# Performance work log

Hardware: AMD Instinct MI355X
Metric: run time of the kernel (lower is better)

## Reference

```python
import jax, jax.numpy as jnp
import numpy as np

VOCAB = 267735
CUTOFFS = [20000, 40000, 200000, VOCAB]   # module appends vocab_size
CUT_ENDS = [0] + CUTOFFS
D_PROJ = 1024
D_EMBED = 1024
DIV_VAL = 4
N_CLUSTERS = len(CUTOFFS) - 1  # 3
SEQ, BSZ = 128, 4


def _logit(x, W, b, proj):
    # x: [i,b,d_proj]; proj: [d_emb,d_proj]; W: [n,d_emb]; b: [n]
    y = jnp.einsum('ibd,ed->ibe', x, proj)
    return jnp.einsum('ibe,ne->ibn', y, W) + b


def setup_inputs() -> dict:
    key = jax.random.key(0)
    ks = jax.random.split(key, 16)
    inp = {}
    inp['hidden'] = jax.random.normal(ks[0], (SEQ, BSZ, D_PROJ), jnp.float32)
    inp['target'] = jax.random.randint(ks[1], (SEQ, BSZ), 0, VOCAB, dtype=jnp.int32)
    inp['cluster_weight'] = jax.random.normal(ks[2], (N_CLUSTERS, D_EMBED), jnp.float32) * 0.02
    inp['cluster_bias'] = jnp.zeros((N_CLUSTERS,), jnp.float32)
    for i in range(len(CUTOFFS)):
        d_emb_i = D_EMBED // DIV_VAL ** i
        n_i = CUT_ENDS[i + 1] - CUT_ENDS[i]
        inp[f'proj{i}'] = jax.random.normal(ks[3 + 3 * i], (d_emb_i, D_PROJ), jnp.float32) * 0.02
        inp[f'W{i}'] = jax.random.normal(ks[4 + 3 * i], (n_i, d_emb_i), jnp.float32) * 0.02
        inp[f'b{i}'] = jnp.zeros((n_i,), jnp.float32)
    return inp


def reference(hidden, target, cluster_weight, cluster_bias,
              proj0, proj1, proj2, proj3,
              W0, W1, W2, W3, b0, b1, b2, b3):
    projs = [proj0, proj1, proj2, proj3]
    Ws = [W0, W1, W2, W3]
    bs = [b0, b1, b2, b3]
    # head: shortlist tokens + one pseudo-token per tail cluster
    head_W = jnp.concatenate([W0, cluster_weight], axis=0)   # [20003, d_embed]
    head_b = jnp.concatenate([b0, cluster_bias], axis=0)
    head_logprob = jax.nn.log_softmax(_logit(hidden, head_W, head_b, proj0), axis=-1)
    out = [head_logprob[..., :CUTOFFS[0]]]
    for i in range(1, len(CUTOFFS)):
        tail_logprob = jax.nn.log_softmax(_logit(hidden, Ws[i], bs[i], projs[i]), axis=-1)
        # P(token) = P(cluster i | head) * P(token | cluster i)
        out.append(head_logprob[..., CUTOFFS[0] + i - 1, None] + tail_logprob)
    out = jnp.concatenate(out, axis=-1)  # [seq, bsz, vocab] full log-probs
    # Per-cluster boolean_mask + gather + scatter_nd in the original is exactly
    # a gather of the concatenated log-prob at the target id.
    tgt_logprob = jnp.take_along_axis(out, target[..., None].astype(jnp.int32), axis=-1)[..., 0]
    loss = -jnp.mean(tgt_logprob)  # return_mean=True
    return out, loss
```

## Files before the change

kernel.cpp:

```cpp
#include <hip/hip_runtime.h>
#include <hip/hip_bf16.h>

#define VOCAB_SZ 267735
#define NROWS 512

typedef __attribute__((ext_vector_type(8))) short bf16x8;
typedef __attribute__((ext_vector_type(4))) float f32x4;

typedef const __attribute__((address_space(1))) unsigned int* gas_u32p;
typedef __attribute__((address_space(3))) unsigned int* las_u32p;

#define GLOAD_LDS16(g, l) \
    __builtin_amdgcn_global_load_lds((gas_u32p)(const void*)(g), (las_u32p)(void*)(l), 16, 0, 0)

enum { MODE_Y = 0, MODE_RW = 1 };

template<int MODE>
__global__ __launch_bounds__(256)
void gemm_k(const __hip_bfloat16* __restrict__ A, int lda, int K,
            const __hip_bfloat16* __restrict__ B,
            int Nmat, int Nsplit,
            const float* __restrict__ bias, const float* __restrict__ bias2,
            float* __restrict__ rowsum,
            float* __restrict__ outp, int Nstore,
            float* __restrict__ clog,
            __hip_bfloat16* __restrict__ yout, int yld, int ywidth)
{
    const int t = threadIdx.x;
    const int col0 = blockIdx.x * 128;
    const int row0 = blockIdx.y * 128;
    const int wid = t >> 6, lane = t & 63, q = lane >> 4, l16 = lane & 15;
    const int wm = wid >> 1, wn = wid & 1;

    __shared__ __hip_bfloat16 sA[128 * 32];
    __shared__ __hip_bfloat16 sB[128 * 32];
    __shared__ float rs[2][128];

    f32x4 acc[4][4];
    f32x4 zf = {0.f, 0.f, 0.f, 0.f};
#pragma unroll
    for (int i = 0; i < 4; i++)
#pragma unroll
        for (int j = 0; j < 4; j++) acc[i][j] = zf;

    const int id0 = t, id1 = 256 + t;
    const __hip_bfloat16* a0 = A + (size_t)(row0 + (id0 >> 2)) * lda + ((id0 & 3) << 3);
    const __hip_bfloat16* a1 = A + (size_t)(row0 + (id1 >> 2)) * lda + ((id1 & 3) << 3);
    const __hip_bfloat16* b0 = B + (size_t)(col0 + (id0 >> 2)) * K + ((id0 & 3) << 3);
    const __hip_bfloat16* b1 = B + (size_t)(col0 + (id1 >> 2)) * K + ((id1 & 3) << 3);
    char* sAb = (char*)sA;
    char* sBb = (char*)sB;
    const bf16x8* sAv = (const bf16x8*)sA;
    const bf16x8* sBv = (const bf16x8*)sB;

    for (int k0 = 0; k0 < K; k0 += 32) {
        __syncthreads();
        GLOAD_LDS16(a0 + k0, sAb + id0 * 16);
        GLOAD_LDS16(a1 + k0, sAb + id1 * 16);
        GLOAD_LDS16(b0 + k0, sBb + id0 * 16);
        GLOAD_LDS16(b1 + k0, sBb + id1 * 16);
        __syncthreads();

        bf16x8 af[4], bfr[4];
#pragma unroll
        for (int i = 0; i < 4; i++) af[i]  = sAv[(wm * 64 + i * 16 + l16) * 4 + q];
#pragma unroll
        for (int j = 0; j < 4; j++) bfr[j] = sBv[(wn * 64 + j * 16 + l16) * 4 + q];
#pragma unroll
        for (int i = 0; i < 4; i++)
#pragma unroll
            for (int j = 0; j < 4; j++)
                acc[i][j] = __builtin_amdgcn_mfma_f32_16x16x32_bf16(af[i], bfr[j], acc[i][j], 0, 0, 0);
    }

    int colg[4];
#pragma unroll
    for (int j = 0; j < 4; j++) colg[j] = col0 + wn * 64 + j * 16 + l16;

    if (MODE == MODE_Y) {
#pragma unroll
        for (int i = 0; i < 4; i++) {
            int rbase = row0 + wm * 64 + i * 16 + q * 4;
#pragma unroll
            for (int j = 0; j < 4; j++) {
                if (colg[j] < ywidth) {
#pragma unroll
                    for (int r = 0; r < 4; r++)
                        yout[(size_t)(rbase + r) * yld + colg[j]] = __float2bfloat16(acc[i][j][r]);
                }
            }
        }
    } else {
        float bv[4]; bool ok[4];
#pragma unroll
        for (int j = 0; j < 4; j++) {
            ok[j] = colg[j] < Nmat;
            bv[j] = colg[j] < Nsplit ? bias[colg[j]] : (ok[j] ? bias2[colg[j] - Nsplit] : 0.f);
        }
#pragma unroll
        for (int i = 0; i < 4; i++) {
            int rbase = row0 + wm * 64 + i * 16 + q * 4;
#pragma unroll
            for (int r = 0; r < 4; r++) {
                int rg = rbase + r;
                float* orow = outp + (size_t)rg * VOCAB_SZ;
                float s = 0.f;
#pragma unroll
                for (int j = 0; j < 4; j++) {
                    if (ok[j]) {
                        float v = acc[i][j][r] + bv[j];
                        s += __expf(v);
                        if (colg[j] < Nstore)
                            __builtin_nontemporal_store(v, orow + colg[j]);
                        else if (clog != nullptr)
                            clog[(colg[j] - Nstore) * NROWS + rg] = v;
                    }
                }
                s += __shfl_xor(s, 1);
                s += __shfl_xor(s, 2);
                s += __shfl_xor(s, 4);
                s += __shfl_xor(s, 8);
                if (l16 == 0) rs[wn][wm * 64 + i * 16 + q * 4 + r] = s;
            }
        }
        __syncthreads();
        if (t < 128) atomicAdd(&rowsum[row0 + t], rs[0][t] + rs[1][t]);
    }
}

__device__ inline void cvt8_store(__hip_bfloat16* dst, const float* src)
{
    float4 f0 = ((const float4*)src)[0];
    float4 f1 = ((const float4*)src)[1];
    __hip_bfloat16 h[8] __attribute__((aligned(16)));
    h[0] = __float2bfloat16(f0.x); h[1] = __float2bfloat16(f0.y);
    h[2] = __float2bfloat16(f0.z); h[3] = __float2bfloat16(f0.w);
    h[4] = __float2bfloat16(f1.x); h[5] = __float2bfloat16(f1.y);
    h[6] = __float2bfloat16(f1.z); h[7] = __float2bfloat16(f1.w);
    *((uint4*)dst) = *((uint4*)h);
}
__device__ inline void zero8_store(__hip_bfloat16* dst)
{
    uint4 z = {0u, 0u, 0u, 0u};
    *((uint4*)dst) = z;
}

__global__ __launch_bounds__(256)
void conv_k(const float* __restrict__ hidden, const float* __restrict__ cw,
            const float* __restrict__ p0, const float* __restrict__ p1,
            const float* __restrict__ p2, const float* __restrict__ p3,
            const float* __restrict__ W0, const float* __restrict__ W1,
            const float* __restrict__ W2, const float* __restrict__ W3,
            __hip_bfloat16* __restrict__ hb, __hip_bfloat16* __restrict__ pj,
            __hip_bfloat16* __restrict__ wb0, __hip_bfloat16* __restrict__ wb1,
            __hip_bfloat16* __restrict__ wb2, __hip_bfloat16* __restrict__ wb3,
            float* __restrict__ rowsum)
{
    const long gid0 = (long)blockIdx.x * 256 + threadIdx.x;
    if (gid0 < 512) ((float4*)rowsum)[gid0] = make_float4(0.f, 0.f, 0.f, 0.f);
    const long stride = (long)gridDim.x * 256;
    for (long c = gid0; c < 5012480L; c += stride) {
        if (c < 65536L)        { long o = c * 8;              cvt8_store(hb + o, hidden + o); }
        else if (c < 196608L)  { long o = (c - 65536L) * 8;   cvt8_store(pj + o, p0 + o); }
        else if (c < 229376L)  { long o = (c - 196608L) * 8;  cvt8_store(pj + 1048576L + o, p1 + o); }
        else if (c < 237568L)  { long o = (c - 229376L) * 8;  cvt8_store(pj + 1310720L + o, p2 + o); }
        else if (c < 239616L)  { long o = (c - 237568L) * 8;  cvt8_store(pj + 1376256L + o, p3 + o); }
        else if (c < 245760L)  { long o = (c - 239616L) * 8;  zero8_store(pj + 1392640L + o); }
        else if (c < 2805760L) { long o = (c - 245760L) * 8;  cvt8_store(wb0 + o, W0 + o); }
        else if (c < 2806144L) { long o = (c - 2805760L) * 8; cvt8_store(wb0 + 20480000L + o, cw + o); }
        else if (c < 2818048L) { long o = (c - 2806144L) * 8; zero8_store(wb0 + 20483072L + o); }
        else if (c < 3458048L) { long o = (c - 2818048L) * 8; cvt8_store(wb1 + o, W1 + o); }
        else if (c < 3461120L) { long o = (c - 3458048L) * 8; zero8_store(wb1 + 5120000L + o); }
        else if (c < 4741120L) { long o = (c - 3461120L) * 8; cvt8_store(wb2 + o, W2 + o); }
        else {
            long o = (c - 4741120L) * 8;
            long row = o >> 5; int col = (int)(o & 31);
            if (row < 67735L && col < 16) cvt8_store(wb3 + o, W3 + row * 16 + col);
            else                          zero8_store(wb3 + o);
        }
    }
}

__global__ void finalize_k(const float* __restrict__ rowsum, const float* __restrict__ clog,
                           float* __restrict__ adj)
{
    int r = threadIdx.x;
    float lse0 = logf(rowsum[r]);
    adj[r]        = -lse0;
    adj[512 + r]  = clog[r]        - lse0 - logf(rowsum[512 + r]);
    adj[1024 + r] = clog[512 + r]  - lse0 - logf(rowsum[1024 + r]);
    adj[1536 + r] = clog[1024 + r] - lse0 - logf(rowsum[1536 + r]);
}

__global__ __launch_bounds__(256)
void fixup_k(float* __restrict__ out, const float* __restrict__ adj)
{
    const int r = blockIdx.y;
    const float a0 = adj[r], a1 = adj[512 + r], a2 = adj[1024 + r], a3 = adj[1536 + r];
    float* row = out + (size_t)r * VOCAB_SZ;
    const int lead = (int)((4u - ((((size_t)row) >> 2) & 3u)) & 3u);
    const int tid = blockIdx.x * 256 + threadIdx.x;
    const int nth = gridDim.x * 256;
    if (blockIdx.x == 0 && threadIdx.x < lead)
        row[threadIdx.x] += a0;
    const int nvec = (VOCAB_SZ - lead) >> 2;
    f32x4* vrow = (f32x4*)(row + lead);
    for (int v = tid; v < nvec; v += nth) {
        const int c = lead + (v << 2);
        f32x4 x = __builtin_nontemporal_load(vrow + v);
        x[0] += (c     < 20000) ? a0 : (c     < 40000) ? a1 : (c     < 200000) ? a2 : a3;
        x[1] += (c + 1 < 20000) ? a0 : (c + 1 < 40000) ? a1 : (c + 1 < 200000) ? a2 : a3;
        x[2] += (c + 2 < 20000) ? a0 : (c + 2 < 40000) ? a1 : (c + 2 < 200000) ? a2 : a3;
        x[3] += (c + 3 < 20000) ? a0 : (c + 3 < 40000) ? a1 : (c + 3 < 200000) ? a2 : a3;
        __builtin_nontemporal_store(x, vrow + v);
    }
    for (int c = lead + (nvec << 2) + tid; c < VOCAB_SZ; c += nth)
        row[c] += a3;
}

__global__ void loss_k(const float* __restrict__ out, const int* __restrict__ tgt,
                       float* __restrict__ lossp)
{
    __shared__ float sm[512];
    int t = threadIdx.x;
    sm[t] = out[(size_t)t * VOCAB_SZ + tgt[t]];
    __syncthreads();
    for (int s = 256; s > 0; s >>= 1) {
        if (t < s) sm[t] += sm[t + s];
        __syncthreads();
    }
    if (t == 0) lossp[0] = -sm[0] / 512.f;
}

extern "C" void kernel_launch(void* const* d_in, const int* in_sizes, int n_in,
                              void* d_out, int out_size, void* d_ws, size_t ws_size,
                              hipStream_t stream)
{
    const float* hidden = (const float*)d_in[0];
    const int*   target = (const int*)d_in[1];
    const float* cw     = (const float*)d_in[2];
    const float* cb     = (const float*)d_in[3];
    const float* proj[4] = {(const float*)d_in[4], (const float*)d_in[7],
                            (const float*)d_in[10], (const float*)d_in[13]};
    const float* W[4]    = {(const float*)d_in[5], (const float*)d_in[8],
                            (const float*)d_in[11], (const float*)d_in[14]};
    const float* bb[4]   = {(const float*)d_in[6], (const float*)d_in[9],
                            (const float*)d_in[12], (const float*)d_in[15]};
    float* out = (float*)d_out;

    char* ws = (char*)d_ws;
    __hip_bfloat16* hb  = (__hip_bfloat16*)ws;
    __hip_bfloat16* y   = (__hip_bfloat16*)(ws + 1048576);
    __hip_bfloat16* pj  = (__hip_bfloat16*)(ws + 2490368);
    __hip_bfloat16* wb0 = (__hip_bfloat16*)(ws + 5373952);
    __hip_bfloat16* wb1 = (__hip_bfloat16*)(ws + 46530560);
    __hip_bfloat16* wb2 = (__hip_bfloat16*)(ws + 56819712);
    __hip_bfloat16* wb3 = (__hip_bfloat16*)(ws + 77299712);
    float* rowsum = (float*)(ws + 81641472);
    float* adj    = (float*)(ws + 81649664);
    float* clog   = (float*)(ws + 81657856);

    conv_k<<<4096, 256, 0, stream>>>(hidden, cw,
        proj[0], proj[1], proj[2], proj[3], W[0], W[1], W[2], W[3],
        hb, pj, wb0, wb1, wb2, wb3, rowsum);

    gemm_k<MODE_Y><<<dim3(11, 4), 256, 0, stream>>>(hb, 1024, 1024, pj,
        1408, 1408, nullptr, nullptr, nullptr, nullptr, 0, nullptr, y, 1408, 1408);

    gemm_k<MODE_RW><<<dim3(157, 4), 256, 0, stream>>>(y, 1408, 1024, wb0,
        20003, 20000, bb[0], cb, rowsum, out, 20000, clog, nullptr, 0, 0);
    gemm_k<MODE_RW><<<dim3(157, 4), 256, 0, stream>>>(y + 1024, 1408, 256, wb1,
        20000, 20000, bb[1], bb[1], rowsum + 512, out + 20000, 20000, nullptr, nullptr, 0, 0);
    gemm_k<MODE_RW><<<dim3(1250, 4), 256, 0, stream>>>(y + 1280, 1408, 64, wb2,
        160000, 160000, bb[2], bb[2], rowsum + 1024, out + 40000, 160000, nullptr, nullptr, 0, 0);
    gemm_k<MODE_RW><<<dim3(530, 4), 256, 0, stream>>>(y + 1344, 1408, 32, wb3,
        67735, 67735, bb[3], bb[3], rowsum + 1536, out + 200000, 67735, nullptr, nullptr, 0, 0);

    finalize_k<<<1, 512, 0, stream>>>(rowsum, clog, adj);

    fixup_k<<<dim3(32, 512), 256, 0, stream>>>(out, adj);

    loss_k<<<1, 512, 0, stream>>>(out, target, out + (out_size - 1));
}
```

Baseline: 1.127 ms.

## Recompute logits in second GEMM pass instead of read-modify-write fixup

The logits GEMMs now run twice. The first pass only accumulates the exp row sums (and the cluster logits), and the second pass recomputes the logits and writes the final log-probs with the per-row adjustment already added. This drops the separate fixup kernel, which read and rewrote the whole 512x267735 fp32 output, in exchange for doubling the cheap low-K matmul work. It also adds double-buffered LDS loads in the GEMM main loop, which removes one barrier per k-step and overlaps global loads with MFMA.

```diff
diff --git a/kernel.cpp b/kernel.cpp
--- a/kernel.cpp
+++ b/kernel.cpp
@@ -13,7 +13,7 @@
 #define GLOAD_LDS16(g, l) \
     __builtin_amdgcn_global_load_lds((gas_u32p)(const void*)(g), (las_u32p)(void*)(l), 16, 0, 0)
 
-enum { MODE_Y = 0, MODE_RW = 1 };
+enum { MODE_Y = 0, MODE_REDUCE = 1, MODE_WRITE = 2 };
 
 template<int MODE>
 __global__ __launch_bounds__(256)
@@ -22,6 +22,7 @@
             int Nmat, int Nsplit,
             const float* __restrict__ bias, const float* __restrict__ bias2,
             float* __restrict__ rowsum,
+            const float* __restrict__ adj,
             float* __restrict__ outp, int Nstore,
             float* __restrict__ clog,
             __hip_bfloat16* __restrict__ yout, int yld, int ywidth)
@@ -32,8 +33,8 @@
     const int wid = t >> 6, lane = t & 63, q = lane >> 4, l16 = lane & 15;
     const int wm = wid >> 1, wn = wid & 1;
 
-    __shared__ __hip_bfloat16 sA[128 * 32];
-    __shared__ __hip_bfloat16 sB[128 * 32];
+    __shared__ __hip_bfloat16 sA[2][128 * 32];
+    __shared__ __hip_bfloat16 sB[2][128 * 32];
     __shared__ float rs[2][128];
 
     f32x4 acc[4][4];
@@ -50,17 +51,40 @@
     const __hip_bfloat16* b1 = B + (size_t)(col0 + (id1 >> 2)) * K + ((id1 & 3) << 3);
     char* sAb = (char*)sA;
     char* sBb = (char*)sB;
-    const bf16x8* sAv = (const bf16x8*)sA;
-    const bf16x8* sBv = (const bf16x8*)sB;
-
-    for (int k0 = 0; k0 < K; k0 += 32) {
+
+    GLOAD_LDS16(a0, sAb + id0 * 16);
+    GLOAD_LDS16(a1, sAb + id1 * 16);
+    GLOAD_LDS16(b0, sBb + id0 * 16);
+    GLOAD_LDS16(b1, sBb + id1 * 16);
+    __syncthreads();
+
+    int cur = 0;
+    for (int k0 = 32; k0 < K; k0 += 32) {
+        const int nxt = cur ^ 1;
+        GLOAD_LDS16(a0 + k0, sAb + nxt * 8192 + id0 * 16);
+        GLOAD_LDS16(a1 + k0, sAb + nxt * 8192 + id1 * 16);
+        GLOAD_LDS16(b0 + k0, sBb + nxt * 8192 + id0 * 16);
+        GLOAD_LDS16(b1 + k0, sBb + nxt * 8192 + id1 * 16);
+
+        const bf16x8* sAv = (const bf16x8*)(sAb + cur * 8192);
+        const bf16x8* sBv = (const bf16x8*)(sBb + cur * 8192);
+        bf16x8 af[4], bfr[4];
+#pragma unroll
+        for (int i = 0; i < 4; i++) af[i]  = sAv[(wm * 64 + i * 16 + l16) * 4 + q];
+#pragma unroll
+        for (int j = 0; j < 4; j++) bfr[j] = sBv[(wn * 64 + j * 16 + l16) * 4 + q];
+#pragma unroll
+        for (int i = 0; i < 4; i++)
+#pragma unroll
+            for (int j = 0; j < 4; j++)
+                acc[i][j] = __builtin_amdgcn_mfma_f32_16x16x32_bf16(af[i], bfr[j], acc[i][j], 0, 0, 0);
+
         __syncthreads();
-        GLOAD_LDS16(a0 + k0, sAb + id0 * 16);
-        GLOAD_LDS16(a1 + k0, sAb + id1 * 16);
-        GLOAD_LDS16(b0 + k0, sBb + id0 * 16);
-        GLOAD_LDS16(b1 + k0, sBb + id1 * 16);
-        __syncthreads();
-
+        cur = nxt;
+    }
+    {
+        const bf16x8* sAv = (const bf16x8*)(sAb + cur * 8192);
+        const bf16x8* sBv = (const bf16x8*)(sBb + cur * 8192);
         bf16x8 af[4], bfr[4];
 #pragma unroll
         for (int i = 0; i < 4; i++) af[i]  = sAv[(wm * 64 + i * 16 + l16) * 4 + q];
@@ -90,7 +114,7 @@
                 }
             }
         }
-    } else {
+    } else if (MODE == MODE_REDUCE) {
         float bv[4]; bool ok[4];
 #pragma unroll
         for (int j = 0; j < 4; j++) {
@@ -103,16 +127,13 @@
 #pragma unroll
             for (int r = 0; r < 4; r++) {
                 int rg = rbase + r;
-                float* orow = outp + (size_t)rg * VOCAB_SZ;
                 float s = 0.f;
 #pragma unroll
                 for (int j = 0; j < 4; j++) {
                     if (ok[j]) {
                         float v = acc[i][j][r] + bv[j];
                         s += __expf(v);
-                        if (colg[j] < Nstore)
-                            __builtin_nontemporal_store(v, orow + colg[j]);
-                        else if (clog != nullptr)
+                        if (clog != nullptr && colg[j] >= Nstore)
                             clog[(colg[j] - Nstore) * NROWS + rg] = v;
                     }
                 }
@@ -125,6 +146,25 @@
         }
         __syncthreads();
         if (t < 128) atomicAdd(&rowsum[row0 + t], rs[0][t] + rs[1][t]);
+    } else {
+        float bv[4];
+#pragma unroll
+        for (int j = 0; j < 4; j++)
+            bv[j] = colg[j] < Nsplit ? bias[colg[j]] : (colg[j] < Nmat ? bias2[colg[j] - Nsplit] : 0.f);
+#pragma unroll
+        for (int i = 0; i < 4; i++) {
+            int rbase = row0 + wm * 64 + i * 16 + q * 4;
+#pragma unroll
+            for (int r = 0; r < 4; r++) {
+                int rg = rbase + r;
+                float av = adj[rg];
+                float* orow = outp + (size_t)rg * VOCAB_SZ;
+#pragma unroll
+                for (int j = 0; j < 4; j++)
+                    if (colg[j] < Nstore)
+                        __builtin_nontemporal_store(acc[i][j][r] + bv[j] + av, orow + colg[j]);
+            }
+        }
     }
 }
 
@@ -192,32 +232,6 @@
     adj[1536 + r] = clog[1024 + r] - lse0 - logf(rowsum[1536 + r]);
 }
 
-__global__ __launch_bounds__(256)
-void fixup_k(float* __restrict__ out, const float* __restrict__ adj)
-{
-    const int r = blockIdx.y;
-    const float a0 = adj[r], a1 = adj[512 + r], a2 = adj[1024 + r], a3 = adj[1536 + r];
-    float* row = out + (size_t)r * VOCAB_SZ;
-    const int lead = (int)((4u - ((((size_t)row) >> 2) & 3u)) & 3u);
-    const int tid = blockIdx.x * 256 + threadIdx.x;
-    const int nth = gridDim.x * 256;
-    if (blockIdx.x == 0 && threadIdx.x < lead)
-        row[threadIdx.x] += a0;
-    const int nvec = (VOCAB_SZ - lead) >> 2;
-    f32x4* vrow = (f32x4*)(row + lead);
-    for (int v = tid; v < nvec; v += nth) {
-        const int c = lead + (v << 2);
-        f32x4 x = __builtin_nontemporal_load(vrow + v);
-        x[0] += (c     < 20000) ? a0 : (c     < 40000) ? a1 : (c     < 200000) ? a2 : a3;
-        x[1] += (c + 1 < 20000) ? a0 : (c + 1 < 40000) ? a1 : (c + 1 < 200000) ? a2 : a3;
-        x[2] += (c + 2 < 20000) ? a0 : (c + 2 < 40000) ? a1 : (c + 2 < 200000) ? a2 : a3;
-        x[3] += (c + 3 < 20000) ? a0 : (c + 3 < 40000) ? a1 : (c + 3 < 200000) ? a2 : a3;
-        __builtin_nontemporal_store(x, vrow + v);
-    }
-    for (int c = lead + (nvec << 2) + tid; c < VOCAB_SZ; c += nth)
-        row[c] += a3;
-}
-
 __global__ void loss_k(const float* __restrict__ out, const int* __restrict__ tgt,
                        float* __restrict__ lossp)
 {
@@ -265,20 +279,27 @@
         hb, pj, wb0, wb1, wb2, wb3, rowsum);
 
     gemm_k<MODE_Y><<<dim3(11, 4), 256, 0, stream>>>(hb, 1024, 1024, pj,
-        1408, 1408, nullptr, nullptr, nullptr, nullptr, 0, nullptr, y, 1408, 1408);
-
-    gemm_k<MODE_RW><<<dim3(157, 4), 256, 0, stream>>>(y, 1408, 1024, wb0,
-        20003, 20000, bb[0], cb, rowsum, out, 20000, clog, nullptr, 0, 0);
-    gemm_k<MODE_RW><<<dim3(157, 4), 256, 0, stream>>>(y + 1024, 1408, 256, wb1,
-        20000, 20000, bb[1], bb[1], rowsum + 512, out + 20000, 20000, nullptr, nullptr, 0, 0);
-    gemm_k<MODE_RW><<<dim3(1250, 4), 256, 0, stream>>>(y + 1280, 1408, 64, wb2,
-        160000, 160000, bb[2], bb[2], rowsum + 1024, out + 40000, 160000, nullptr, nullptr, 0, 0);
-    gemm_k<MODE_RW><<<dim3(530, 4), 256, 0, stream>>>(y + 1344, 1408, 32, wb3,
-        67735, 67735, bb[3], bb[3], rowsum + 1536, out + 200000, 67735, nullptr, nullptr, 0, 0);
+        1408, 1408, nullptr, nullptr, nullptr, nullptr, nullptr, 0, nullptr, y, 1408, 1408);
+
+    gemm_k<MODE_REDUCE><<<dim3(157, 4), 256, 0, stream>>>(y, 1408, 1024, wb0,
+        20003, 20000, bb[0], cb, rowsum, nullptr, nullptr, 20000, clog, nullptr, 0, 0);
+    gemm_k<MODE_REDUCE><<<dim3(157, 4), 256, 0, stream>>>(y + 1024, 1408, 256, wb1,
+        20000, 20000, bb[1], bb[1], rowsum + 512, nullptr, nullptr, 20000, nullptr, nullptr, 0, 0);
+    gemm_k<MODE_REDUCE><<<dim3(1250, 4), 256, 0, stream>>>(y + 1280, 1408, 64, wb2,
+        160000, 160000, bb[2], bb[2], rowsum + 1024, nullptr, nullptr, 160000, nullptr, nullptr, 0, 0);
+    gemm_k<MODE_REDUCE><<<dim3(530, 4), 256, 0, stream>>>(y + 1344, 1408, 32, wb3,
+        67735, 67735, bb[3], bb[3], rowsum + 1536, nullptr, nullptr, 67735, nullptr, nullptr, 0, 0);
 
     finalize_k<<<1, 512, 0, stream>>>(rowsum, clog, adj);
 
-    fixup_k<<<dim3(32, 512), 256, 0, stream>>>(out, adj);
+    gemm_k<MODE_WRITE><<<dim3(157, 4), 256, 0, stream>>>(y, 1408, 1024, wb0,
+        20003, 20000, bb[0], cb, nullptr, adj, out, 20000, nullptr, nullptr, 0, 0);
+    gemm_k<MODE_WRITE><<<dim3(157, 4), 256, 0, stream>>>(y + 1024, 1408, 256, wb1,
+        20000, 20000, bb[1], bb[1], nullptr, adj + 512, out + 20000, 20000, nullptr, nullptr, 0, 0);
+    gemm_k<MODE_WRITE><<<dim3(1250, 4), 256, 0, stream>>>(y + 1280, 1408, 64, wb2,
+        160000, 160000, bb[2], bb[2], nullptr, adj + 1024, out + 40000, 160000, nullptr, nullptr, 0, 0);
+    gemm_k<MODE_WRITE><<<dim3(530, 4), 256, 0, stream>>>(y + 1344, 1408, 32, wb3,
+        67735, 67735, bb[3], bb[3], nullptr, adj + 1536, out + 200000, 67735, nullptr, nullptr, 0, 0);
 
     loss_k<<<1, 512, 0, stream>>>(out, target, out + (out_size - 1));
 }
```

Result: slower. 1.375 ms (+22.0%).
